# Optimization experiments

Measured on AMD Instinct MI355X. Metric: run time of the kernel, lower is better.

## Reference

```python
import jax, jax.numpy as jnp
import numpy as np

N_NODES = 100000
N_EDGES = 1000000
D_FEAT = 64          # per-node embedding dim
IN_FEATS = 2 * D_FEAT  # concat(src, dst)
HID = 128


def setup_inputs() -> dict:
    key = jax.random.key(0)
    ks = jax.random.split(key, 12)
    zi = jax.random.normal(ks[0], (N_NODES, D_FEAT), dtype=jnp.float32)
    zj = jax.random.normal(ks[1], (N_NODES, D_FEAT), dtype=jnp.float32)
    zn = jax.random.normal(ks[2], (N_NODES, D_FEAT), dtype=jnp.float32)
    pos_src = jax.random.randint(ks[3], (N_EDGES,), 0, N_NODES)
    pos_dst = jax.random.randint(ks[4], (N_EDGES,), 0, N_NODES)
    neg_src = jax.random.randint(ks[5], (N_EDGES,), 0, N_NODES)
    neg_dst = jax.random.randint(ks[6], (N_EDGES,), 0, N_NODES)
    # MLP params (nn.Linear style: y = x @ W.T + b)
    s1 = 1.0 / np.sqrt(IN_FEATS)
    s3 = 1.0 / np.sqrt(HID)
    W1 = jax.random.uniform(ks[7], (HID, IN_FEATS), jnp.float32, -s1, s1)
    b1 = jax.random.uniform(ks[8], (HID,), jnp.float32, -s1, s1)
    W3 = jax.random.uniform(ks[9], (1, HID), jnp.float32, -s3, s3)
    b3 = jax.random.uniform(ks[10], (1,), jnp.float32, -s3, s3)
    return {"zi": zi, "zj": zj, "zn": zn, "W1": W1, "b1": b1, "W3": W3,
            "b3": b3, "pos_src": pos_src, "pos_dst": pos_dst,
            "neg_src": neg_src, "neg_dst": neg_dst}


def _lp(raw, W1, b1, W3, b3):
    # Link_Prediction with n_layers=2, dropout=0: linear-relu-linear-sigmoid
    hid = jax.nn.relu(raw @ W1.T + b1)      # [E, HID]
    return jax.nn.sigmoid(hid @ W3.T + b3)  # [E, 1]


def reference(zi, zj, zn, W1, b1, W3, b3, pos_src, pos_dst, neg_src, neg_dst):
    # pos graph: gather src/dst node embeddings per edge, concat -> MLP
    raw_pos = jnp.concatenate([zi[pos_src], zj[pos_dst]], axis=1)  # [E, 2*D]
    pos_score = _lp(raw_pos, W1, b1, W3, b3)
    # NOTE: source bug — neg score is computed from the POS raw features
    # (pos_graph.edata['raw']); the neg gather/concat is dead code, so we
    # faithfully score raw_pos again.
    neg_score = _lp(raw_pos, W1, b1, W3, b3)
    return pos_score, neg_score
```

## Files before the change

kernel.cpp:

```cpp
#include <hip/hip_runtime.h>
#include <hip/hip_fp8.h>

typedef float    f32x16 __attribute__((ext_vector_type(16)));
typedef _Float16 f16x8  __attribute__((ext_vector_type(8)));

#define NWAVES 4
#define TPW 4
#define TILES_PER_BLOCK (NWAVES * TPW)

__device__ __forceinline__ uint32_t enc4_fp8(float a, float b, float c, float d) {
#if __has_builtin(__builtin_amdgcn_cvt_pk_fp8_f32)
    int w = __builtin_amdgcn_cvt_pk_fp8_f32(a, b, 0, false);
    w     = __builtin_amdgcn_cvt_pk_fp8_f32(c, d, w, true);
    return (uint32_t)w;
#else
    __hip_fp8_e4m3 e0(a), e1(b), e2(c), e3(d);
    return (uint32_t)e0.__x | ((uint32_t)e1.__x << 8) |
           ((uint32_t)e2.__x << 16) | ((uint32_t)e3.__x << 24);
#endif
}

__device__ __forceinline__ void dec4_fp8(uint32_t w, _Float16* o) {
#if __has_builtin(__builtin_amdgcn_cvt_pk_f32_fp8)
    const auto f01 = __builtin_amdgcn_cvt_pk_f32_fp8((int)w, false);
    const auto f23 = __builtin_amdgcn_cvt_pk_f32_fp8((int)w, true);
    const auto h01 = __builtin_amdgcn_cvt_pkrtz(f01[0], f01[1]);
    const auto h23 = __builtin_amdgcn_cvt_pkrtz(f23[0], f23[1]);
    o[0] = h01[0]; o[1] = h01[1]; o[2] = h23[0]; o[3] = h23[1];
#else
    #pragma unroll
    for (int j = 0; j < 4; ++j) {
        __hip_fp8_e4m3 t; t.__x = (unsigned char)(w >> (8 * j));
        o[j] = (_Float16)(float)t;
    }
#endif
}

__device__ __forceinline__ f16x8 dec8_fp8(uint2 u) {
    f16x8 v;
    _Float16 tmp[8];
    dec4_fp8(u.x, tmp);
    dec4_fp8(u.y, tmp + 4);
    #pragma unroll
    for (int j = 0; j < 8; ++j) v[j] = tmp[j];
    return v;
}

__global__ __launch_bounds__(256) void prep_fp8(
    const float* __restrict__ zi, const float* __restrict__ zj,
    uint2* __restrict__ zif8, uint2* __restrict__ zjf8, const int nChunkPer)
{
    const int stride = gridDim.x * blockDim.x;
    for (int c = blockIdx.x * blockDim.x + threadIdx.x; c < 2 * nChunkPer; c += stride) {
        const float* s;
        uint2* d;
        int cc;
        if (c < nChunkPer) { cc = c; s = zi + (size_t)cc * 8; d = zif8 + cc; }
        else { cc = c - nChunkPer; s = zj + (size_t)cc * 8; d = zjf8 + cc; }
        const float4 a0 = *reinterpret_cast<const float4*>(s);
        const float4 a1 = *reinterpret_cast<const float4*>(s + 4);
        uint2 w;
        w.x = enc4_fp8(a0.x, a0.y, a0.z, a0.w);
        w.y = enc4_fp8(a1.x, a1.y, a1.z, a1.w);
        *d = w;
    }
}

template<bool FP8>
__global__ __launch_bounds__(256) void graphlp_mfma(
    const float* __restrict__ zi, const float* __restrict__ zj,
    const unsigned char* __restrict__ zif8, const unsigned char* __restrict__ zjf8,
    const float* __restrict__ W1, const float* __restrict__ b1p,
    const float* __restrict__ W3, const float* __restrict__ b3p,
    const int* __restrict__ psrc, const int* __restrict__ pdst,
    float* __restrict__ out, const int nEdges, const int nTiles)
{
    __shared__ uint4 w1s[2048];
    char* lds = reinterpret_cast<char*>(w1s);
    const int tid = threadIdx.x;

    #pragma unroll
    for (int i = 0; i < 8; ++i) {
        const int ch  = tid + i * 256;
        const int row = ch >> 4;
        const int kg  = ch & 15;
        const float* s = W1 + row * 128 + kg * 8;
        const float4 a0 = *reinterpret_cast<const float4*>(s);
        const float4 a1 = *reinterpret_cast<const float4*>(s + 4);
        f16x8 v;
        v[0]=(_Float16)a0.x; v[1]=(_Float16)a0.y; v[2]=(_Float16)a0.z; v[3]=(_Float16)a0.w;
        v[4]=(_Float16)a1.x; v[5]=(_Float16)a1.y; v[6]=(_Float16)a1.z; v[7]=(_Float16)a1.w;
        const int off = row * 256 + ((kg * 16) ^ ((row & 7) << 4));
        *reinterpret_cast<f16x8*>(lds + off) = v;
    }
    __syncthreads();

    const int lane = tid & 63;
    const int wav  = tid >> 6;
    const int lr   = lane & 31;
    const int lq   = lane >> 5;

    float b1v[4], w3v[4];
    #pragma unroll
    for (int nb = 0; nb < 4; ++nb) {
        b1v[nb] = b1p[nb * 32 + lr];
        w3v[nb] = W3[nb * 32 + lr];
    }
    const float b3 = b3p[0];

    int si = 0, di = 0;
    {
        const int g0 = blockIdx.x * TILES_PER_BLOCK + wav;
        if (g0 < nTiles) {
            const int e = min(g0 * 32 + lr, nEdges - 1);
            si = psrc[e]; di = pdst[e];
        }
    }

    #pragma unroll
    for (int t = 0; t < TPW; ++t) {
        const int g = blockIdx.x * TILES_PER_BLOCK + t * NWAVES + wav;
        if (g >= nTiles) break;

        int si_n = 0, di_n = 0;
        if (t + 1 < TPW) {
            const int gn = g + NWAVES;
            if (gn < nTiles) {
                const int en = min(gn * 32 + lr, nEdges - 1);
                si_n = psrc[en]; di_n = pdst[en];
            }
        }

        f16x8 afrag[8];
        if constexpr (FP8) {
            const unsigned char* __restrict__ sp = zif8 + (size_t)si * 64;
            const unsigned char* __restrict__ dp = zjf8 + (size_t)di * 64;
            uint2 px[8];
            #pragma unroll
            for (int kk = 0; kk < 4; ++kk) {
                px[kk]     = *reinterpret_cast<const uint2*>(sp + kk * 16 + lq * 8);
                px[kk + 4] = *reinterpret_cast<const uint2*>(dp + kk * 16 + lq * 8);
            }
            #pragma unroll
            for (int kk = 0; kk < 8; ++kk) afrag[kk] = dec8_fp8(px[kk]);
        } else {
            const float* __restrict__ sp = zi + (size_t)si * 64;
            const float* __restrict__ dp = zj + (size_t)di * 64;
            #pragma unroll
            for (int kk = 0; kk < 8; ++kk) {
                const int kb = kk * 16 + lq * 8;
                const float* p = (kk < 4) ? (sp + kb) : (dp + kb - 64);
                const float4 a0 = *reinterpret_cast<const float4*>(p);
                const float4 a1 = *reinterpret_cast<const float4*>(p + 4);
                f16x8 v;
                v[0]=(_Float16)a0.x; v[1]=(_Float16)a0.y; v[2]=(_Float16)a0.z; v[3]=(_Float16)a0.w;
                v[4]=(_Float16)a1.x; v[5]=(_Float16)a1.y; v[6]=(_Float16)a1.z; v[7]=(_Float16)a1.w;
                afrag[kk] = v;
            }
        }

        float pr[16];
        #pragma unroll
        for (int r = 0; r < 16; ++r) pr[r] = 0.0f;

        #pragma unroll
        for (int nbp = 0; nbp < 2; ++nbp) {
            const float bb0 = b1v[2*nbp], bb1 = b1v[2*nbp + 1];
            f32x16 acc0, acc1;
            #pragma unroll
            for (int r = 0; r < 16; ++r) { acc0[r] = bb0; acc1[r] = bb1; }
            const int n0 = (2*nbp)     * 32 + lr;
            const int n1 = (2*nbp + 1) * 32 + lr;
            __builtin_amdgcn_s_setprio(1);
            #pragma unroll
            for (int kk = 0; kk < 8; ++kk) {
                const int kx = kk * 32 + lq * 16;
                const f16x8 bf0 = *reinterpret_cast<const f16x8*>(
                    lds + n0 * 256 + (kx ^ ((n0 & 7) << 4)));
                const f16x8 bf1 = *reinterpret_cast<const f16x8*>(
                    lds + n1 * 256 + (kx ^ ((n1 & 7) << 4)));
                acc0 = __builtin_amdgcn_mfma_f32_32x32x16_f16(afrag[kk], bf0, acc0, 0, 0, 0);
                acc1 = __builtin_amdgcn_mfma_f32_32x32x16_f16(afrag[kk], bf1, acc1, 0, 0, 0);
            }
            __builtin_amdgcn_s_setprio(0);
            const float ww0 = w3v[2*nbp], ww1 = w3v[2*nbp + 1];
            #pragma unroll
            for (int r = 0; r < 16; ++r) {
                pr[r] = fmaf(fmaxf(acc0[r], 0.0f), ww0, pr[r]);
                pr[r] = fmaf(fmaxf(acc1[r], 0.0f), ww1, pr[r]);
            }
        }

        float p8[8];
        #pragma unroll
        for (int r = 0; r < 8; ++r) {
            const float lo = pr[r], hi = pr[r + 8];
            const float sent = (lane & 1) ? lo : hi;
            const float got  = __shfl_xor(sent, 1);
            p8[r] = ((lane & 1) ? hi : lo) + got;
        }
        float p4[4];
        #pragma unroll
        for (int r = 0; r < 4; ++r) {
            const float lo = p8[r], hi = p8[r + 4];
            const float sent = (lane & 2) ? lo : hi;
            const float got  = __shfl_xor(sent, 2);
            p4[r] = ((lane & 2) ? hi : lo) + got;
        }
        float p2[2];
        #pragma unroll
        for (int r = 0; r < 2; ++r) {
            const float lo = p4[r], hi = p4[r + 2];
            const float sent = (lane & 4) ? lo : hi;
            const float got  = __shfl_xor(sent, 4);
            p2[r] = ((lane & 4) ? hi : lo) + got;
        }
        float p1;
        {
            const float lo = p2[0], hi = p2[1];
            const float sent = (lane & 8) ? lo : hi;
            const float got  = __shfl_xor(sent, 8);
            p1 = ((lane & 8) ? hi : lo) + got;
        }
        p1 += __shfl_xor(p1, 16);

        const int rid = 8 * (lane & 1) + 4 * ((lane >> 1) & 1)
                      + 2 * ((lane >> 2) & 1) + ((lane >> 3) & 1);
        const int m  = (rid & 3) + 8 * (rid >> 2) + 4 * lq;
        const int eo = g * 32 + m;
        if (eo < nEdges) {
            const float sc = 1.0f / (1.0f + __expf(-(p1 + b3)));
            if (lane & 16) out[nEdges + eo] = sc;
            else           out[eo] = sc;
        }

        si = si_n; di = di_n;
    }
}

extern "C" void kernel_launch(void* const* d_in, const int* in_sizes, int n_in,
                              void* d_out, int out_size, void* d_ws, size_t ws_size,
                              hipStream_t stream)
{
    const float* zi = (const float*)d_in[0];
    const float* zj = (const float*)d_in[1];
    const float* W1 = (const float*)d_in[3];
    const float* b1 = (const float*)d_in[4];
    const float* W3 = (const float*)d_in[5];
    const float* b3 = (const float*)d_in[6];
    const int* psrc = (const int*)d_in[7];
    const int* pdst = (const int*)d_in[8];
    float* out = (float*)d_out;

    const int nEdges = in_sizes[7];
    const int nNodesI = in_sizes[0] / 64;
    const int nNodesJ = in_sizes[1] / 64;
    const int nTiles = (nEdges + 31) / 32;
    const int nBlocks = (nTiles + TILES_PER_BLOCK - 1) / TILES_PER_BLOCK;

    const size_t bytesI = (size_t)nNodesI * 64;
    const size_t bytesJ = (size_t)nNodesJ * 64;
    const bool useF8 = (ws_size >= bytesI + bytesJ);

    if (useF8) {
        unsigned char* zif8 = (unsigned char*)d_ws;
        unsigned char* zjf8 = (unsigned char*)d_ws + bytesI;
        const int nChunkPer = nNodesI * 64 / 8;
        hipLaunchKernelGGL(prep_fp8, dim3(2048), dim3(256), 0, stream,
                           zi, zj, (uint2*)zif8, (uint2*)zjf8, nChunkPer);
        hipLaunchKernelGGL((graphlp_mfma<true>), dim3(nBlocks), dim3(256), 0, stream,
                           zi, zj, zif8, zjf8, W1, b1, W3, b3, psrc, pdst,
                           out, nEdges, nTiles);
    } else {
        hipLaunchKernelGGL((graphlp_mfma<false>), dim3(nBlocks), dim3(256), 0, stream,
                           zi, zj, (const unsigned char*)nullptr, (const unsigned char*)nullptr,
                           W1, b1, W3, b3, psrc, pdst, out, nEdges, nTiles);
    }
}
```

Measured before the change: 72.36 us.

## Use native FP8 MFMA with split hi/residual FP8 weights instead of FP16

Measured after the change: 71.67 us. No clear change (-1.0%).

```diff
diff --git a/kernel.cpp b/kernel.cpp
--- a/kernel.cpp
+++ b/kernel.cpp
@@ -3,6 +3,7 @@
 
 typedef float    f32x16 __attribute__((ext_vector_type(16)));
 typedef _Float16 f16x8  __attribute__((ext_vector_type(8)));
+typedef long     i64;
 
 #define NWAVES 4
 #define TPW 4
@@ -20,30 +21,22 @@
 #endif
 }
 
-__device__ __forceinline__ void dec4_fp8(uint32_t w, _Float16* o) {
+__device__ __forceinline__ void dec4_fp8f(uint32_t w, float* o) {
 #if __has_builtin(__builtin_amdgcn_cvt_pk_f32_fp8)
     const auto f01 = __builtin_amdgcn_cvt_pk_f32_fp8((int)w, false);
     const auto f23 = __builtin_amdgcn_cvt_pk_f32_fp8((int)w, true);
-    const auto h01 = __builtin_amdgcn_cvt_pkrtz(f01[0], f01[1]);
-    const auto h23 = __builtin_amdgcn_cvt_pkrtz(f23[0], f23[1]);
-    o[0] = h01[0]; o[1] = h01[1]; o[2] = h23[0]; o[3] = h23[1];
+    o[0] = f01[0]; o[1] = f01[1]; o[2] = f23[0]; o[3] = f23[1];
 #else
     #pragma unroll
     for (int j = 0; j < 4; ++j) {
         __hip_fp8_e4m3 t; t.__x = (unsigned char)(w >> (8 * j));
-        o[j] = (_Float16)(float)t;
+        o[j] = (float)t;
     }
 #endif
 }
 
-__device__ __forceinline__ f16x8 dec8_fp8(uint2 u) {
-    f16x8 v;
-    _Float16 tmp[8];
-    dec4_fp8(u.x, tmp);
-    dec4_fp8(u.y, tmp + 4);
-    #pragma unroll
-    for (int j = 0; j < 8; ++j) v[j] = tmp[j];
-    return v;
+__device__ __forceinline__ i64 mk64(uint32_t lo, uint32_t hi) {
+    return (i64)(((unsigned long long)hi << 32) | (unsigned long long)lo);
 }
 
 __global__ __launch_bounds__(256) void prep_fp8(
@@ -66,10 +59,35 @@
     }
 }
 
+__global__ __launch_bounds__(256) void prep_w1(
+    const float* __restrict__ W1, uint4* __restrict__ w1pack)
+{
+    const int c = blockIdx.x * blockDim.x + threadIdx.x;
+    if (c >= 2048) return;
+    const int n  = c >> 4, q = c & 15;
+    const int kk = q >> 1, lq = q & 1;
+    const int kbase = (kk < 4) ? (lq * 32 + kk * 8) : (64 + lq * 32 + (kk - 4) * 8);
+    const float* w = W1 + n * 128 + kbase;
+    const float4 w0 = *reinterpret_cast<const float4*>(w);
+    const float4 w1 = *reinterpret_cast<const float4*>(w + 4);
+    const uint32_t h0 = enc4_fp8(w0.x, w0.y, w0.z, w0.w);
+    const uint32_t h1 = enc4_fp8(w1.x, w1.y, w1.z, w1.w);
+    float d0[4], d1[4];
+    dec4_fp8f(h0, d0);
+    dec4_fp8f(h1, d1);
+    const uint32_t r0 = enc4_fp8((w0.x - d0[0]) * 16.0f, (w0.y - d0[1]) * 16.0f,
+                                 (w0.z - d0[2]) * 16.0f, (w0.w - d0[3]) * 16.0f);
+    const uint32_t r1 = enc4_fp8((w1.x - d1[0]) * 16.0f, (w1.y - d1[1]) * 16.0f,
+                                 (w1.z - d1[2]) * 16.0f, (w1.w - d1[3]) * 16.0f);
+    uint4 o; o.x = h0; o.y = h1; o.z = r0; o.w = r1;
+    w1pack[c] = o;
+}
+
 template<bool FP8>
 __global__ __launch_bounds__(256) void graphlp_mfma(
     const float* __restrict__ zi, const float* __restrict__ zj,
     const unsigned char* __restrict__ zif8, const unsigned char* __restrict__ zjf8,
+    const uint4* __restrict__ w1pack,
     const float* __restrict__ W1, const float* __restrict__ b1p,
     const float* __restrict__ W3, const float* __restrict__ b3p,
     const int* __restrict__ psrc, const int* __restrict__ pdst,
@@ -79,19 +97,31 @@
     char* lds = reinterpret_cast<char*>(w1s);
     const int tid = threadIdx.x;
 
-    #pragma unroll
-    for (int i = 0; i < 8; ++i) {
-        const int ch  = tid + i * 256;
-        const int row = ch >> 4;
-        const int kg  = ch & 15;
-        const float* s = W1 + row * 128 + kg * 8;
-        const float4 a0 = *reinterpret_cast<const float4*>(s);
-        const float4 a1 = *reinterpret_cast<const float4*>(s + 4);
-        f16x8 v;
-        v[0]=(_Float16)a0.x; v[1]=(_Float16)a0.y; v[2]=(_Float16)a0.z; v[3]=(_Float16)a0.w;
-        v[4]=(_Float16)a1.x; v[5]=(_Float16)a1.y; v[6]=(_Float16)a1.z; v[7]=(_Float16)a1.w;
-        const int off = row * 256 + ((kg * 16) ^ ((row & 7) << 4));
-        *reinterpret_cast<f16x8*>(lds + off) = v;
+    if constexpr (FP8) {
+        #pragma unroll
+        for (int i = 0; i < 8; ++i) {
+            const int ch = tid + i * 256;
+            const int n  = ch >> 4;
+            const int q  = ch & 15;
+            const uint4 v = w1pack[ch];
+            const int off = n * 256 + ((q * 16) ^ ((n & 7) << 4));
+            *reinterpret_cast<uint4*>(lds + off) = v;
+        }
+    } else {
+        #pragma unroll
+        for (int i = 0; i < 8; ++i) {
+            const int ch  = tid + i * 256;
+            const int row = ch >> 4;
+            const int kg  = ch & 15;
+            const float* s = W1 + row * 128 + kg * 8;
+            const float4 a0 = *reinterpret_cast<const float4*>(s);
+            const float4 a1 = *reinterpret_cast<const float4*>(s + 4);
+            f16x8 v;
+            v[0]=(_Float16)a0.x; v[1]=(_Float16)a0.y; v[2]=(_Float16)a0.z; v[3]=(_Float16)a0.w;
+            v[4]=(_Float16)a1.x; v[5]=(_Float16)a1.y; v[6]=(_Float16)a1.z; v[7]=(_Float16)a1.w;
+            const int off = row * 256 + ((kg * 16) ^ ((row & 7) << 4));
+            *reinterpret_cast<f16x8*>(lds + off) = v;
+        }
     }
     __syncthreads();
 
@@ -117,7 +147,6 @@
         }
     }
 
-    #pragma unroll
     for (int t = 0; t < TPW; ++t) {
         const int g = blockIdx.x * TILES_PER_BLOCK + t * NWAVES + wav;
         if (g >= nTiles) break;
@@ -131,19 +160,52 @@
             }
         }
 
-        f16x8 afrag[8];
+        float pr[16];
+        #pragma unroll
+        for (int r = 0; r < 16; ++r) pr[r] = 0.0f;
+
         if constexpr (FP8) {
             const unsigned char* __restrict__ sp = zif8 + (size_t)si * 64;
             const unsigned char* __restrict__ dp = zjf8 + (size_t)di * 64;
-            uint2 px[8];
+            const uint4 as0 = *reinterpret_cast<const uint4*>(sp + lq * 32);
+            const uint4 as1 = *reinterpret_cast<const uint4*>(sp + lq * 32 + 16);
+            const uint4 ad0 = *reinterpret_cast<const uint4*>(dp + lq * 32);
+            const uint4 ad1 = *reinterpret_cast<const uint4*>(dp + lq * 32 + 16);
+            i64 aop[8];
+            aop[0] = mk64(as0.x, as0.y); aop[1] = mk64(as0.z, as0.w);
+            aop[2] = mk64(as1.x, as1.y); aop[3] = mk64(as1.z, as1.w);
+            aop[4] = mk64(ad0.x, ad0.y); aop[5] = mk64(ad0.z, ad0.w);
+            aop[6] = mk64(ad1.x, ad1.y); aop[7] = mk64(ad1.z, ad1.w);
+
             #pragma unroll
-            for (int kk = 0; kk < 4; ++kk) {
-                px[kk]     = *reinterpret_cast<const uint2*>(sp + kk * 16 + lq * 8);
-                px[kk + 4] = *reinterpret_cast<const uint2*>(dp + kk * 16 + lq * 8);
+            for (int nb = 0; nb < 4; ++nb) {
+                const float bb = b1v[nb];
+                f32x16 acc, accr;
+                #pragma unroll
+                for (int r = 0; r < 16; ++r) { acc[r] = bb; accr[r] = 0.0f; }
+                const int n   = nb * 32 + lr;
+                const int nsw = (n & 7) << 4;
+                const int nbase = n * 256;
+                __builtin_amdgcn_s_setprio(1);
+                #pragma unroll
+                for (int kk = 0; kk < 8; ++kk) {
+                    const int off = nbase + (((kk * 2 + lq) * 16) ^ nsw);
+                    const uint4 w = *reinterpret_cast<const uint4*>(lds + off);
+                    acc  = __builtin_amdgcn_mfma_f32_32x32x16_fp8_fp8(
+                               aop[kk], mk64(w.x, w.y), acc,  0, 0, 0);
+                    accr = __builtin_amdgcn_mfma_f32_32x32x16_fp8_fp8(
+                               aop[kk], mk64(w.z, w.w), accr, 0, 0, 0);
+                }
+                __builtin_amdgcn_s_setprio(0);
+                const float ww = w3v[nb];
+                #pragma unroll
+                for (int r = 0; r < 16; ++r) {
+                    const float h = fmaf(accr[r], 0.0625f, acc[r]);
+                    pr[r] = fmaf(fmaxf(h, 0.0f), ww, pr[r]);
+                }
             }
-            #pragma unroll
-            for (int kk = 0; kk < 8; ++kk) afrag[kk] = dec8_fp8(px[kk]);
         } else {
+            f16x8 afrag[8];
             const float* __restrict__ sp = zi + (size_t)si * 64;
             const float* __restrict__ dp = zj + (size_t)di * 64;
             #pragma unroll
@@ -157,37 +219,30 @@
                 v[4]=(_Float16)a1.x; v[5]=(_Float16)a1.y; v[6]=(_Float16)a1.z; v[7]=(_Float16)a1.w;
                 afrag[kk] = v;
             }
-        }
-
-        float pr[16];
-        #pragma unroll
-        for (int r = 0; r < 16; ++r) pr[r] = 0.0f;
-
-        #pragma unroll
-        for (int nbp = 0; nbp < 2; ++nbp) {
-            const float bb0 = b1v[2*nbp], bb1 = b1v[2*nbp + 1];
-            f32x16 acc0, acc1;
             #pragma unroll
-            for (int r = 0; r < 16; ++r) { acc0[r] = bb0; acc1[r] = bb1; }
-            const int n0 = (2*nbp)     * 32 + lr;
-            const int n1 = (2*nbp + 1) * 32 + lr;
-            __builtin_amdgcn_s_setprio(1);
-            #pragma unroll
-            for (int kk = 0; kk < 8; ++kk) {
-                const int kx = kk * 32 + lq * 16;
-                const f16x8 bf0 = *reinterpret_cast<const f16x8*>(
-                    lds + n0 * 256 + (kx ^ ((n0 & 7) << 4)));
-                const f16x8 bf1 = *reinterpret_cast<const f16x8*>(
-                    lds + n1 * 256 + (kx ^ ((n1 & 7) << 4)));
-                acc0 = __builtin_amdgcn_mfma_f32_32x32x16_f16(afrag[kk], bf0, acc0, 0, 0, 0);
-                acc1 = __builtin_amdgcn_mfma_f32_32x32x16_f16(afrag[kk], bf1, acc1, 0, 0, 0);
-            }
-            __builtin_amdgcn_s_setprio(0);
-            const float ww0 = w3v[2*nbp], ww1 = w3v[2*nbp + 1];
-            #pragma unroll
-            for (int r = 0; r < 16; ++r) {
-                pr[r] = fmaf(fmaxf(acc0[r], 0.0f), ww0, pr[r]);
-                pr[r] = fmaf(fmaxf(acc1[r], 0.0f), ww1, pr[r]);
+            for (int nbp = 0; nbp < 2; ++nbp) {
+                const float bb0 = b1v[2*nbp], bb1 = b1v[2*nbp + 1];
+                f32x16 acc0, acc1;
+                #pragma unroll
+                for (int r = 0; r < 16; ++r) { acc0[r] = bb0; acc1[r] = bb1; }
+                const int n0 = (2*nbp)     * 32 + lr;
+                const int n1 = (2*nbp + 1) * 32 + lr;
+                #pragma unroll
+                for (int kk = 0; kk < 8; ++kk) {
+                    const int kx = kk * 32 + lq * 16;
+                    const f16x8 bf0 = *reinterpret_cast<const f16x8*>(
+                        lds + n0 * 256 + (kx ^ ((n0 & 7) << 4)));
+                    const f16x8 bf1 = *reinterpret_cast<const f16x8*>(
+                        lds + n1 * 256 + (kx ^ ((n1 & 7) << 4)));
+                    acc0 = __builtin_amdgcn_mfma_f32_32x32x16_f16(afrag[kk], bf0, acc0, 0, 0, 0);
+                    acc1 = __builtin_amdgcn_mfma_f32_32x32x16_f16(afrag[kk], bf1, acc1, 0, 0, 0);
+                }
+                const float ww0 = w3v[2*nbp], ww1 = w3v[2*nbp + 1];
+                #pragma unroll
+                for (int r = 0; r < 16; ++r) {
+                    pr[r] = fmaf(fmaxf(acc0[r], 0.0f), ww0, pr[r]);
+                    pr[r] = fmaf(fmaxf(acc1[r], 0.0f), ww1, pr[r]);
+                }
             }
         }
 
@@ -260,20 +315,24 @@
 
     const size_t bytesI = (size_t)nNodesI * 64;
     const size_t bytesJ = (size_t)nNodesJ * 64;
-    const bool useF8 = (ws_size >= bytesI + bytesJ);
+    const size_t bytesW = 2048 * 16;
+    const bool useF8 = (ws_size >= bytesI + bytesJ + bytesW);
 
     if (useF8) {
         unsigned char* zif8 = (unsigned char*)d_ws;
         unsigned char* zjf8 = (unsigned char*)d_ws + bytesI;
+        uint4* w1pack = (uint4*)((unsigned char*)d_ws + bytesI + bytesJ);
         const int nChunkPer = nNodesI * 64 / 8;
         hipLaunchKernelGGL(prep_fp8, dim3(2048), dim3(256), 0, stream,
                            zi, zj, (uint2*)zif8, (uint2*)zjf8, nChunkPer);
+        hipLaunchKernelGGL(prep_w1, dim3(8), dim3(256), 0, stream, W1, w1pack);
         hipLaunchKernelGGL((graphlp_mfma<true>), dim3(nBlocks), dim3(256), 0, stream,
-                           zi, zj, zif8, zjf8, W1, b1, W3, b3, psrc, pdst,
+                           zi, zj, zif8, zjf8, w1pack, W1, b1, W3, b3, psrc, pdst,
                            out, nEdges, nTiles);
     } else {
         hipLaunchKernelGGL((graphlp_mfma<false>), dim3(nBlocks), dim3(256), 0, stream,
                            zi, zj, (const unsigned char*)nullptr, (const unsigned char*)nullptr,
-                           W1, b1, W3, b3, psrc, pdst, out, nEdges, nTiles);
-    }
-}
+                           (const uint4*)nullptr, W1, b1, W3, b3, psrc, pdst,
+                           out, nEdges, nTiles);
+    }
+}
```
